# Performance work log

Measured on AMD Instinct MI355X. Metric: run time of the kernel, lower is better.

Reference implementation:

```python
import jax, jax.numpy as jnp
import numpy as np

T, H, I, E, K = 4096, 2048, 1408, 8, 2


def setup_inputs() -> dict:
    key = jax.random.key(0)
    k1, k2, k3, k4, k5 = jax.random.split(key, 5)
    hidden_states = jax.random.normal(k1, (T, H), dtype=jnp.float32)
    w13 = jax.random.normal(k2, (E, 2 * I, H), dtype=jnp.float32) * 0.02
    w2 = jax.random.normal(k3, (E, H, I), dtype=jnp.float32) * 0.02
    topk_ids = jax.random.randint(k4, (T, K), 0, E, dtype=jnp.int32)
    topk_weights = jax.random.uniform(k5, (T, K), dtype=jnp.float32)
    return {
        "hidden_states": hidden_states,
        "w13": w13,
        "w2": w2,
        "topk_ids": topk_ids,
        "topk_weights": topk_weights,
    }


def reference(hidden_states, w13, w2, topk_ids, topk_weights):
    # hidden_states: [T, H]; w13: [E, 2I, H]; w2: [E, H, I]
    # topk_ids/topk_weights: [T, K]. local_expert_start = 0.
    num_tokens, hidden = hidden_states.shape
    num_experts = w13.shape[0]
    inter = w13.shape[1] // 2
    gate_w = w13[:, :inter, :]  # [E, I, H]
    up_w = w13[:, inter:, :]    # [E, I, H]

    # Dense per-expert gate/up projections (vectorized grouped GEMM).
    gate = jnp.einsum('th,eih->tei', hidden_states, gate_w)
    up = jnp.einsum('th,eih->tei', hidden_states, up_w)
    act = jax.nn.silu(gate) * up  # [T, E, I]

    # Scatter topk weights into a dense [T, E] routing matrix (zero elsewhere),
    # which reproduces the trivial impl's per-slot weighted accumulation.
    tok = jnp.arange(num_tokens, dtype=jnp.int32)[:, None]
    routing = jnp.zeros((num_tokens, num_experts), dtype=hidden_states.dtype)
    routing = routing.at[tok, topk_ids].add(topk_weights)

    # Weighted combine through the down projection; weighting act first avoids
    # materializing a [T, E, H] intermediate.
    act_w = act * routing[:, :, None]  # [T, E, I]
    out = jnp.einsum('tei,ehi->th', act_w, w2)  # [T, H]
    return out
```

## Files before the change

kernel.cpp:

```cpp
#include <hip/hip_runtime.h>
#include <hip/hip_bf16.h>

#define T_TOK 4096
#define HID   2048
#define INTER 1408
#define TWO_I 2816
#define NEXP  8
#define ROWCAP 9216

#define N8_HS  1048576
#define N8_W13 5767168
#define NCVT   ((N8_HS + N8_W13) / 256)

using bf16x8 = __attribute__((ext_vector_type(8))) __bf16;
using f32x4  = __attribute__((ext_vector_type(4))) float;

__device__ __forceinline__ unsigned short f2bf(float f) {
  unsigned u = __float_as_uint(f);
  u += 0x7fffu + ((u >> 16) & 1u);
  return (unsigned short)(u >> 16);
}

__device__ __forceinline__ void gload16(const void* g, void* l) {
  __builtin_amdgcn_global_load_lds(
      (const __attribute__((address_space(1))) void*)g,
      (__attribute__((address_space(3))) void*)l, 16, 0, 0);
}

__device__ __forceinline__ uint4 pack8(float4 a, float4 b) {
  union { unsigned short us[8]; uint4 v; } o;
  o.us[0] = f2bf(a.x); o.us[1] = f2bf(a.y); o.us[2] = f2bf(a.z); o.us[3] = f2bf(a.w);
  o.us[4] = f2bf(b.x); o.us[5] = f2bf(b.y); o.us[6] = f2bf(b.z); o.us[7] = f2bf(b.w);
  return o.v;
}

__global__ void cvt2route_kernel(const float* __restrict__ hs_f, unsigned short* __restrict__ hs_b,
                                 const float* __restrict__ w13_f, unsigned short* __restrict__ w13_b,
                                 const int* __restrict__ ids, const float* __restrict__ wts,
                                 float* __restrict__ R, int* __restrict__ counts) {
  int bid = blockIdx.x;
  if (bid >= NCVT) {
    int t = (bid - NCVT) * 256 + threadIdx.x;
    if (t >= T_TOK) return;
    int e0 = ids[t * 2], e1 = ids[t * 2 + 1];
    float w0 = wts[t * 2], w1 = wts[t * 2 + 1];
#pragma unroll
    for (int ee = 0; ee < NEXP; ++ee) {
      float r = (e0 == ee ? w0 : 0.0f) + (e1 == ee ? w1 : 0.0f);
      R[t * NEXP + ee] = r;
    }
    atomicAdd(&counts[e0], 1);
    if (e1 != e0) atomicAdd(&counts[e1], 1);
    return;
  }
  int i = bid * 256 + threadIdx.x;
  const float4* p;
  uint4* o;
  int j;
  if (i < N8_HS) {
    p = reinterpret_cast<const float4*>(hs_f);
    o = reinterpret_cast<uint4*>(hs_b);
    j = i;
  } else {
    p = reinterpret_cast<const float4*>(w13_f);
    o = reinterpret_cast<uint4*>(w13_b);
    j = i - N8_HS;
  }
  o[j] = pack8(p[j * 2], p[j * 2 + 1]);
}

__global__ void offsets_kernel(const int* __restrict__ counts,
                               int* __restrict__ offs, int* __restrict__ cursor,
                               int* __restrict__ tl) {
  if (threadIdx.x == 0) {
    int o = 0;
    for (int e = 0; e < NEXP; ++e) {
      offs[e] = o;
      cursor[e] = o;
      o += (counts[e] + 127) & ~127;
    }
    offs[NEXP] = o;
  }
  for (int i = threadIdx.x; i < ROWCAP; i += 256) tl[i] = -1;
}

__global__ void scatter_kernel(const int* __restrict__ ids,
                               int* __restrict__ cursor, int* __restrict__ tl,
                               int* __restrict__ inv) {
  int t = blockIdx.x * 256 + threadIdx.x;
  if (t >= T_TOK) return;
  int e0 = ids[t * 2], e1 = ids[t * 2 + 1];
  int p = atomicAdd(&cursor[e0], 1);
  tl[p] = t;
  inv[t * 2] = p;
  if (e1 != e0) {
    p = atomicAdd(&cursor[e1], 1);
    tl[p] = t;
    inv[t * 2 + 1] = p;
  } else {
    inv[t * 2 + 1] = -1;
  }
}


#define BARR do { __asm__ __volatile__("" ::: "memory"); \
                  __builtin_amdgcn_s_barrier();           \
                  __asm__ __volatile__("" ::: "memory"); } while (0)
#define VMC(n) __asm__ __volatile__("s_waitcnt vmcnt(" #n ")" ::: "memory")

#define STG(P, h, kt, slotOff, hOff)                                        \
  do {                                                                      \
    gload16(P[h][0] + (kt) * 128, smem + (slotOff) + (hOff) + chA);         \
    gload16(P[h][1] + (kt) * 128, smem + (slotOff) + (hOff) + chA + 1024);  \
  } while (0)

#define LDA(dst, S, aq)                                                     \
  do {                                                                      \
    _Pragma("unroll") for (int mi = 0; mi < 4; ++mi) {                      \
      const char* _p = smem + (S) + wmOff + ((aq) * 64 + mi * 16 + l15) * 128; \
      dst[mi][0] = *(const bf16x8*)(_p + ko0);                              \
      dst[mi][1] = *(const bf16x8*)(_p + ko1);                              \
    }                                                                       \
  } while (0)

#define LDB(dst, S, bq)                                                     \
  do {                                                                      \
    _Pragma("unroll") for (int ni = 0; ni < 2; ++ni) {                      \
      const char* _p = smem + (S) + 32768 + wnhOff +                        \
                       (wn1 * 64 + ((bq) * 2 + ni) * 16 + l15) * 128;       \
      dst[ni][0] = *(const bf16x8*)(_p + ko0);                              \
      dst[ni][1] = *(const bf16x8*)(_p + ko1);                              \
    }                                                                       \
  } while (0)

#define MFQ(A, B, aq, bq)                                                   \
  do {                                                                      \
    __builtin_amdgcn_s_setprio(1);                                          \
    _Pragma("unroll") for (int mi = 0; mi < 4; ++mi)                        \
    _Pragma("unroll") for (int ni = 0; ni < 2; ++ni) {                      \
      acc[(aq) * 4 + mi][(bq) * 2 + ni] = __builtin_amdgcn_mfma_f32_16x16x32_bf16( \
          A[mi][0], B[ni][0], acc[(aq) * 4 + mi][(bq) * 2 + ni], 0, 0, 0);  \
      acc[(aq) * 4 + mi][(bq) * 2 + ni] = __builtin_amdgcn_mfma_f32_16x16x32_bf16( \
          A[mi][1], B[ni][1], acc[(aq) * 4 + mi][(bq) * 2 + ni], 0, 0, 0);  \
    }                                                                       \
    __builtin_amdgcn_s_setprio(0);                                          \
  } while (0)

#define EIGHT_PHASES(NIT_, NL_LIM_)                                         \
  for (int i = 0; i < (NIT_); ++i) {                                        \
    const int t0 = 2 * i, t1 = t0 + 1;                                      \
    const bool nl = (i < (NL_LIM_));                                        \
                                                                    \
    LDA(a_lo, 0, 0);                                                        \
    LDB(b_lo, 0, 0);                                                        \
    STG(aS, 0, t1, 65536, 0);                                               \
    BARR; MFQ(a_lo, b_lo, 0, 0); BARR;                                      \
                                                                    \
    LDB(b_hi, 0, 1);                                                        \
    STG(aS, 1, t1, 65536, 16384);                                           \
    BARR; MFQ(a_lo, b_hi, 0, 1); BARR;                                      \
                                                                    \
    LDA(a_hi, 0, 1);                                                        \
    if (nl) STG(bS, 0, t0 + 2, 0, 32768);                                   \
    BARR; MFQ(a_hi, b_hi, 1, 1); BARR;                                      \
                                                                    \
    if (nl) STG(bS, 1, t0 + 2, 0, 49152);                                   \
    BARR; MFQ(a_hi, b_lo, 1, 0);                                            \
    if (nl) { VMC(4); } else { VMC(0); }                                    \
    BARR;                                                                   \
                                                                    \
    LDA(a_lo, 65536, 0);                                                    \
    LDB(b_lo, 65536, 0);                                                    \
    if (nl) STG(aS, 0, t0 + 2, 0, 0);                                       \
    BARR; MFQ(a_lo, b_lo, 0, 0); BARR;                                      \
                                                                    \
    LDB(b_hi, 65536, 1);                                                    \
    if (nl) STG(aS, 1, t0 + 2, 0, 16384);                                   \
    BARR; MFQ(a_lo, b_hi, 0, 1); BARR;                                      \
                                                                    \
    LDA(a_hi, 65536, 1);                                                    \
    if (nl) STG(bS, 0, t1 + 2, 65536, 32768);                               \
    BARR; MFQ(a_hi, b_hi, 1, 1); BARR;                                      \
                                                                    \
    if (nl) STG(bS, 1, t1 + 2, 65536, 49152);                               \
    BARR; MFQ(a_hi, b_lo, 1, 0);                                            \
    if (nl) VMC(4);                                                         \
    BARR;                                                                   \
  }

#define PROLOGUE_STAGE()                                                    \
  do {                                                                      \
    STG(aS, 0, 0, 0, 0);                                                    \
    STG(aS, 1, 0, 0, 16384);                                                \
    STG(bS, 0, 0, 0, 32768);                                                \
    STG(bS, 1, 0, 0, 49152);                                                \
    STG(bS, 0, 1, 65536, 32768);                                            \
    STG(bS, 1, 1, 65536, 49152);                                            \
    VMC(4);                                                                 \
    BARR;                                                                   \
  } while (0)

__global__ __launch_bounds__(512, 2) void gemm1_kernel(
    const unsigned short* __restrict__ hs,
    const unsigned short* __restrict__ w13,
    unsigned short* __restrict__ act,
    const int* __restrict__ tl, const int* __restrict__ offs,
    const float* __restrict__ w2f, unsigned short* __restrict__ w2b) {
  const int tid = threadIdx.x;
  const int lin = blockIdx.x + 11 * (blockIdx.y + 16 * blockIdx.z);

  {
    const float4* p = reinterpret_cast<const float4*>(w2f);
    uint4* o = reinterpret_cast<uint4*>(w2b);
    int gid = lin * 512 + tid;
#pragma unroll
    for (int q = 0; q < 4; ++q) {
      int idx = q * 720896 + gid;
      o[idx] = pack8(p[idx * 2], p[idx * 2 + 1]);
    }
  }

  const int work = (lin & 7) * 176 + (lin >> 3);
  const int bz = work / 176;
  const int rem = work - bz * 176;
  const int bx = rem % 11;
  const int by = rem / 11;

  const int e = bz;
  const int rbeg = offs[e], rend = offs[e + 1];
  const int m0 = rbeg + by * 256;
  if (m0 >= rend) return;
  const int n0 = bx * 128;

  __shared__ __align__(16) char smem[131072];

  const int lane = tid & 63, wave = tid >> 6;
  const int wm = wave >> 2, wn = wave & 3;
  const int l15 = lane & 15;
  const int srow = lane >> 3;
  const int scolswz = ((lane & 7) * 16) ^ (srow << 4);
  const int chA = wave * 2048;
  const int wmOff = wm * 16384;
  const int wnhOff = (wn >> 1) * 16384;
  const int wn1 = wn & 1;
  const int rsw = (lane & 7) << 4;
  const int ko0 = ((lane >> 4) * 16) ^ rsw;
  const int ko1 = (64 + (lane >> 4) * 16) ^ rsw;

  const char* hs_b = (const char*)hs;
  const char* w13_b = (const char*)w13 + (size_t)e * (TWO_I * HID * 2);

  const char* aS[2][2];
  const char* bS[2][2];
#pragma unroll
  for (int h = 0; h < 2; ++h)
#pragma unroll
    for (int it = 0; it < 2; ++it) {
      int rl = h * 128 + (wave * 2 + it) * 8 + srow;
      int grow = m0 + rl;
      int tk = (grow < rend) ? tl[grow] : 0;
      if (tk < 0) tk = 0;
      aS[h][it] = hs_b + (size_t)tk * 4096 + scolswz;
      int wg = rl >> 6, sub = rl & 63;
      int srcB = (sub < 32) ? (n0 + wg * 32 + sub)
                            : (INTER + n0 + wg * 32 + (sub - 32));
      bS[h][it] = w13_b + (size_t)srcB * 4096 + scolswz;
    }

  f32x4 acc[8][4] = {};
  bf16x8 a_lo[4][2], a_hi[4][2], b_lo[2][2], b_hi[2][2];

  PROLOGUE_STAGE();
  EIGHT_PHASES(16, 15);

  const bool okst = (wm == 0) || (rend - m0 >= 256);
  if (okst) {
#pragma unroll
    for (int MI = 0; MI < 8; ++MI)
#pragma unroll
      for (int j = 0; j < 4; ++j) {
        int row = m0 + wm * 128 + MI * 16 + (lane >> 4) * 4 + j;
        size_t base = (size_t)row * INTER + n0 + wn * 32;
#pragma unroll
        for (int NI = 0; NI < 2; ++NI) {
          float g = acc[MI][NI][j], u = acc[MI][NI + 2][j];
          float s = (g / (1.0f + __expf(-g))) * u;
          act[base + NI * 16 + l15] = f2bf(s);
        }
      }
  }
}

__global__ __launch_bounds__(512, 2) void gemm2_kernel(
    const unsigned short* __restrict__ act,
    const unsigned short* __restrict__ w2,
    const float* __restrict__ R, const int* __restrict__ tl,
    const int* __restrict__ offs, unsigned short* __restrict__ partial) {
  const int tid = threadIdx.x;
  const int lin = blockIdx.x + 8 * (blockIdx.y + 16 * blockIdx.z);
  const int work = (lin & 7) * 128 + (lin >> 3);
  const int bz = work >> 7;
  const int rem = work & 127;
  const int bx = rem & 7;
  const int by = rem >> 3;

  const int e = bz;
  const int rbeg = offs[e], rend = offs[e + 1];
  const int m0 = rbeg + by * 256;
  if (m0 >= rend) return;
  const int n0 = bx * 256;

  __shared__ __align__(16) char smem[131072];

  const int lane = tid & 63, wave = tid >> 6;
  const int wm = wave >> 2, wn = wave & 3;
  const int l15 = lane & 15;
  const int srow = lane >> 3;
  const int scolswz = ((lane & 7) * 16) ^ (srow << 4);
  const int chA = wave * 2048;
  const int wmOff = wm * 16384;
  const int wnhOff = (wn >> 1) * 16384;
  const int wn1 = wn & 1;
  const int rsw = (lane & 7) << 4;
  const int ko0 = ((lane >> 4) * 16) ^ rsw;
  const int ko1 = (64 + (lane >> 4) * 16) ^ rsw;

  const char* act_b = (const char*)act;
  const char* w2_b = (const char*)w2 + (size_t)e * (HID * INTER * 2);

  const char* aS[2][2];
  const char* bS[2][2];
#pragma unroll
  for (int h = 0; h < 2; ++h)
#pragma unroll
    for (int it = 0; it < 2; ++it) {
      int rl = h * 128 + (wave * 2 + it) * 8 + srow;
      int grow = m0 + rl;
      if (grow >= rend) grow = rbeg;
      aS[h][it] = act_b + (size_t)grow * (INTER * 2) + scolswz;
      bS[h][it] = w2_b + (size_t)(n0 + rl) * (INTER * 2) + scolswz;
    }

  f32x4 acc[8][4] = {};
  bf16x8 a_lo[4][2], a_hi[4][2], b_lo[2][2], b_hi[2][2];

  PROLOGUE_STAGE();
  EIGHT_PHASES(11, 10);

  const bool okst = (wm == 0) || (rend - m0 >= 256);
  if (okst) {
#pragma unroll
    for (int MI = 0; MI < 8; ++MI) {
      float sc[4];
#pragma unroll
      for (int j = 0; j < 4; ++j) {
        int row = m0 + wm * 128 + MI * 16 + (lane >> 4) * 4 + j;
        int t = tl[row];
        sc[j] = t >= 0 ? R[t * NEXP + e] : 0.0f;
      }
#pragma unroll
      for (int NI = 0; NI < 4; ++NI) {
        int col = n0 + wn * 64 + NI * 16 + l15;
#pragma unroll
        for (int j = 0; j < 4; ++j) {
          int row = m0 + wm * 128 + MI * 16 + (lane >> 4) * 4 + j;
          partial[(size_t)row * HID + col] = f2bf(acc[MI][NI][j] * sc[j]);
        }
      }
    }
  }
}

__global__ void combine_kernel(const unsigned short* __restrict__ P,
                               const int* __restrict__ inv,
                               float* __restrict__ out) {
  int idx = blockIdx.x * 256 + threadIdx.x;
  int t = idx >> 8;
  int c = (idx & 255) << 3;
  int p0 = inv[t * 2], p1 = inv[t * 2 + 1];
  union { uint4 v; unsigned short us[8]; } a, b;
  a.v = *(const uint4*)(P + (size_t)p0 * HID + c);
  float f[8];
#pragma unroll
  for (int j = 0; j < 8; ++j) f[j] = __uint_as_float((unsigned)a.us[j] << 16);
  if (p1 >= 0) {
    b.v = *(const uint4*)(P + (size_t)p1 * HID + c);
#pragma unroll
    for (int j = 0; j < 8; ++j) f[j] += __uint_as_float((unsigned)b.us[j] << 16);
  }
  float4 lo = {f[0], f[1], f[2], f[3]}, hi = {f[4], f[5], f[6], f[7]};
  *(float4*)(out + (size_t)t * HID + c) = lo;
  *(float4*)(out + (size_t)t * HID + c + 4) = hi;
}

extern "C" void kernel_launch(void* const* d_in, const int* in_sizes, int n_in,
                              void* d_out, int out_size, void* d_ws, size_t ws_size,
                              hipStream_t stream) {
  const float* hs_f  = (const float*)d_in[0];
  const float* w13_f = (const float*)d_in[1];
  const float* w2_f  = (const float*)d_in[2];
  const int*   ids   = (const int*)d_in[3];
  const float* wts   = (const float*)d_in[4];
  float* out = (float*)d_out;
  char* ws = (char*)d_ws;

  unsigned short* hs_b  = (unsigned short*)(ws);
  unsigned short* w13_b = (unsigned short*)(ws + 16777216);
  unsigned short* w2_b  = (unsigned short*)(ws + 109051904);
  unsigned short* act   = (unsigned short*)(ws + 155189248);
  float* R              = (float*)(ws + 181141504);
  int*   tl             = (int*)(ws + 181272576);
  int*   inv            = (int*)(ws + 181309440);
  int*   meta           = (int*)(ws + 181342208);
  unsigned short* partial = (unsigned short*)(ws + 16777216);
  int* counts = meta;
  int* offs   = meta + 8;
  int* cursor = meta + 17;

  hipMemsetAsync(meta, 0, 32 * sizeof(int), stream);

  cvt2route_kernel<<<dim3(NCVT + 16), dim3(256), 0, stream>>>(
      hs_f, hs_b, w13_f, w13_b, ids, wts, R, counts);

  offsets_kernel<<<dim3(1), dim3(256), 0, stream>>>(counts, offs, cursor, tl);
  scatter_kernel<<<dim3(T_TOK / 256), dim3(256), 0, stream>>>(ids, cursor, tl, inv);

  gemm1_kernel<<<dim3(11, 16, 8), dim3(512), 0, stream>>>(hs_b, w13_b, act, tl, offs, w2_f, w2_b);
  gemm2_kernel<<<dim3(8, 16, 8), dim3(512), 0, stream>>>(act, w2_b, R, tl, offs, partial);
  combine_kernel<<<dim3(T_TOK * (HID / 8) / 256), dim3(256), 0, stream>>>(partial, inv, out);
}
```

Measured before the change: 299.6 us.

## Use persistent GEMM blocks with an atomic work queue for tile scheduling

Both grouped GEMM kernels now launch 256 persistent blocks instead of one block per potential tile. Each block pulls tile indices from a global atomic counter and skips tiles that lie past an expert's row range. This avoids launching and retiring the many empty tiles and balances work dynamically. The w2 fp32-to-bf16 conversion is redistributed over the 256 blocks. In exchange it adds two barriers per job, loses the previous expert-interleaved tile ordering (jobs now go in expert-major order), and may lower occupancy headroom.

```diff
diff --git a/kernel.cpp b/kernel.cpp
--- a/kernel.cpp
+++ b/kernel.cpp
@@ -11,6 +11,9 @@
 #define N8_HS  1048576
 #define N8_W13 5767168
 #define NCVT   ((N8_HS + N8_W13) / 256)
+
+#define NJOBS1 1408
+#define NJOBS2 1024
 
 using bf16x8 = __attribute__((ext_vector_type(8))) __bf16;
 using f32x4  = __attribute__((ext_vector_type(4))) float;
@@ -205,34 +208,23 @@
     const unsigned short* __restrict__ w13,
     unsigned short* __restrict__ act,
     const int* __restrict__ tl, const int* __restrict__ offs,
-    const float* __restrict__ w2f, unsigned short* __restrict__ w2b) {
+    const float* __restrict__ w2f, unsigned short* __restrict__ w2b,
+    int* __restrict__ qcnt) {
   const int tid = threadIdx.x;
-  const int lin = blockIdx.x + 11 * (blockIdx.y + 16 * blockIdx.z);
 
   {
     const float4* p = reinterpret_cast<const float4*>(w2f);
     uint4* o = reinterpret_cast<uint4*>(w2b);
-    int gid = lin * 512 + tid;
-#pragma unroll
-    for (int q = 0; q < 4; ++q) {
-      int idx = q * 720896 + gid;
+    int gid = blockIdx.x * 512 + tid;
+#pragma unroll
+    for (int q = 0; q < 22; ++q) {
+      int idx = q * 131072 + gid;
       o[idx] = pack8(p[idx * 2], p[idx * 2 + 1]);
     }
   }
 
-  const int work = (lin & 7) * 176 + (lin >> 3);
-  const int bz = work / 176;
-  const int rem = work - bz * 176;
-  const int bx = rem % 11;
-  const int by = rem / 11;
-
-  const int e = bz;
-  const int rbeg = offs[e], rend = offs[e + 1];
-  const int m0 = rbeg + by * 256;
-  if (m0 >= rend) return;
-  const int n0 = bx * 128;
-
   __shared__ __align__(16) char smem[131072];
+  __shared__ int sjob;
 
   const int lane = tid & 63, wave = tid >> 6;
   const int wm = wave >> 2, wn = wave & 3;
@@ -248,46 +240,65 @@
   const int ko1 = (64 + (lane >> 4) * 16) ^ rsw;
 
   const char* hs_b = (const char*)hs;
-  const char* w13_b = (const char*)w13 + (size_t)e * (TWO_I * HID * 2);
-
-  const char* aS[2][2];
-  const char* bS[2][2];
-#pragma unroll
-  for (int h = 0; h < 2; ++h)
-#pragma unroll
-    for (int it = 0; it < 2; ++it) {
-      int rl = h * 128 + (wave * 2 + it) * 8 + srow;
-      int grow = m0 + rl;
-      int tk = (grow < rend) ? tl[grow] : 0;
-      if (tk < 0) tk = 0;
-      aS[h][it] = hs_b + (size_t)tk * 4096 + scolswz;
-      int wg = rl >> 6, sub = rl & 63;
-      int srcB = (sub < 32) ? (n0 + wg * 32 + sub)
-                            : (INTER + n0 + wg * 32 + (sub - 32));
-      bS[h][it] = w13_b + (size_t)srcB * 4096 + scolswz;
+
+  for (;;) {
+    if (tid == 0) sjob = atomicAdd(qcnt, 1);
+    __syncthreads();
+    const int job = sjob;
+    __syncthreads();
+    if (job >= NJOBS1) break;
+
+    const int e = job / 176;
+    const int rem = job - e * 176;
+    const int by = rem / 11;
+    const int bx = rem - by * 11;
+
+    const int rbeg = offs[e], rend = offs[e + 1];
+    const int m0 = rbeg + by * 256;
+    if (m0 >= rend) continue;
+    const int n0 = bx * 128;
+
+    const char* w13_b = (const char*)w13 + (size_t)e * (TWO_I * HID * 2);
+
+    const char* aS[2][2];
+    const char* bS[2][2];
+#pragma unroll
+    for (int h = 0; h < 2; ++h)
+#pragma unroll
+      for (int it = 0; it < 2; ++it) {
+        int rl = h * 128 + (wave * 2 + it) * 8 + srow;
+        int grow = m0 + rl;
+        int tk = (grow < rend) ? tl[grow] : 0;
+        if (tk < 0) tk = 0;
+        aS[h][it] = hs_b + (size_t)tk * 4096 + scolswz;
+        int wg = rl >> 6, sub = rl & 63;
+        int srcB = (sub < 32) ? (n0 + wg * 32 + sub)
+                              : (INTER + n0 + wg * 32 + (sub - 32));
+        bS[h][it] = w13_b + (size_t)srcB * 4096 + scolswz;
+      }
+
+    f32x4 acc[8][4] = {};
+    bf16x8 a_lo[4][2], a_hi[4][2], b_lo[2][2], b_hi[2][2];
+
+    PROLOGUE_STAGE();
+    EIGHT_PHASES(16, 15);
+
+    const bool okst = (wm == 0) || (rend - m0 >= 256);
+    if (okst) {
+#pragma unroll
+      for (int MI = 0; MI < 8; ++MI)
+#pragma unroll
+        for (int j = 0; j < 4; ++j) {
+          int row = m0 + wm * 128 + MI * 16 + (lane >> 4) * 4 + j;
+          size_t base = (size_t)row * INTER + n0 + wn * 32;
+#pragma unroll
+          for (int NI = 0; NI < 2; ++NI) {
+            float g = acc[MI][NI][j], u = acc[MI][NI + 2][j];
+            float s = (g / (1.0f + __expf(-g))) * u;
+            act[base + NI * 16 + l15] = f2bf(s);
+          }
+        }
     }
-
-  f32x4 acc[8][4] = {};
-  bf16x8 a_lo[4][2], a_hi[4][2], b_lo[2][2], b_hi[2][2];
-
-  PROLOGUE_STAGE();
-  EIGHT_PHASES(16, 15);
-
-  const bool okst = (wm == 0) || (rend - m0 >= 256);
-  if (okst) {
-#pragma unroll
-    for (int MI = 0; MI < 8; ++MI)
-#pragma unroll
-      for (int j = 0; j < 4; ++j) {
-        int row = m0 + wm * 128 + MI * 16 + (lane >> 4) * 4 + j;
-        size_t base = (size_t)row * INTER + n0 + wn * 32;
-#pragma unroll
-        for (int NI = 0; NI < 2; ++NI) {
-          float g = acc[MI][NI][j], u = acc[MI][NI + 2][j];
-          float s = (g / (1.0f + __expf(-g))) * u;
-          act[base + NI * 16 + l15] = f2bf(s);
-        }
-      }
   }
 }
 
@@ -295,22 +306,12 @@
     const unsigned short* __restrict__ act,
     const unsigned short* __restrict__ w2,
     const float* __restrict__ R, const int* __restrict__ tl,
-    const int* __restrict__ offs, unsigned short* __restrict__ partial) {
+    const int* __restrict__ offs, unsigned short* __restrict__ partial,
+    int* __restrict__ qcnt) {
   const int tid = threadIdx.x;
-  const int lin = blockIdx.x + 8 * (blockIdx.y + 16 * blockIdx.z);
-  const int work = (lin & 7) * 128 + (lin >> 3);
-  const int bz = work >> 7;
-  const int rem = work & 127;
-  const int bx = rem & 7;
-  const int by = rem >> 3;
-
-  const int e = bz;
-  const int rbeg = offs[e], rend = offs[e + 1];
-  const int m0 = rbeg + by * 256;
-  if (m0 >= rend) return;
-  const int n0 = bx * 256;
 
   __shared__ __align__(16) char smem[131072];
+  __shared__ int sjob;
 
   const int lane = tid & 63, wave = tid >> 6;
   const int wm = wave >> 2, wn = wave & 3;
@@ -326,45 +327,64 @@
   const int ko1 = (64 + (lane >> 4) * 16) ^ rsw;
 
   const char* act_b = (const char*)act;
-  const char* w2_b = (const char*)w2 + (size_t)e * (HID * INTER * 2);
-
-  const char* aS[2][2];
-  const char* bS[2][2];
-#pragma unroll
-  for (int h = 0; h < 2; ++h)
-#pragma unroll
-    for (int it = 0; it < 2; ++it) {
-      int rl = h * 128 + (wave * 2 + it) * 8 + srow;
-      int grow = m0 + rl;
-      if (grow >= rend) grow = rbeg;
-      aS[h][it] = act_b + (size_t)grow * (INTER * 2) + scolswz;
-      bS[h][it] = w2_b + (size_t)(n0 + rl) * (INTER * 2) + scolswz;
-    }
-
-  f32x4 acc[8][4] = {};
-  bf16x8 a_lo[4][2], a_hi[4][2], b_lo[2][2], b_hi[2][2];
-
-  PROLOGUE_STAGE();
-  EIGHT_PHASES(11, 10);
-
-  const bool okst = (wm == 0) || (rend - m0 >= 256);
-  if (okst) {
-#pragma unroll
-    for (int MI = 0; MI < 8; ++MI) {
-      float sc[4];
-#pragma unroll
-      for (int j = 0; j < 4; ++j) {
-        int row = m0 + wm * 128 + MI * 16 + (lane >> 4) * 4 + j;
-        int t = tl[row];
-        sc[j] = t >= 0 ? R[t * NEXP + e] : 0.0f;
+
+  for (;;) {
+    if (tid == 0) sjob = atomicAdd(qcnt, 1);
+    __syncthreads();
+    const int job = sjob;
+    __syncthreads();
+    if (job >= NJOBS2) break;
+
+    const int e = job >> 7;
+    const int rem = job & 127;
+    const int by = rem >> 3;
+    const int bx = rem & 7;
+
+    const int rbeg = offs[e], rend = offs[e + 1];
+    const int m0 = rbeg + by * 256;
+    if (m0 >= rend) continue;
+    const int n0 = bx * 256;
+
+    const char* w2_b = (const char*)w2 + (size_t)e * (HID * INTER * 2);
+
+    const char* aS[2][2];
+    const char* bS[2][2];
+#pragma unroll
+    for (int h = 0; h < 2; ++h)
+#pragma unroll
+      for (int it = 0; it < 2; ++it) {
+        int rl = h * 128 + (wave * 2 + it) * 8 + srow;
+        int grow = m0 + rl;
+        if (grow >= rend) grow = rbeg;
+        aS[h][it] = act_b + (size_t)grow * (INTER * 2) + scolswz;
+        bS[h][it] = w2_b + (size_t)(n0 + rl) * (INTER * 2) + scolswz;
       }
-#pragma unroll
-      for (int NI = 0; NI < 4; ++NI) {
-        int col = n0 + wn * 64 + NI * 16 + l15;
+
+    f32x4 acc[8][4] = {};
+    bf16x8 a_lo[4][2], a_hi[4][2], b_lo[2][2], b_hi[2][2];
+
+    PROLOGUE_STAGE();
+    EIGHT_PHASES(11, 10);
+
+    const bool okst = (wm == 0) || (rend - m0 >= 256);
+    if (okst) {
+#pragma unroll
+      for (int MI = 0; MI < 8; ++MI) {
+        float sc[4];
 #pragma unroll
         for (int j = 0; j < 4; ++j) {
           int row = m0 + wm * 128 + MI * 16 + (lane >> 4) * 4 + j;
-          partial[(size_t)row * HID + col] = f2bf(acc[MI][NI][j] * sc[j]);
+          int t = tl[row];
+          sc[j] = t >= 0 ? R[t * NEXP + e] : 0.0f;
+        }
+#pragma unroll
+        for (int NI = 0; NI < 4; ++NI) {
+          int col = n0 + wn * 64 + NI * 16 + l15;
+#pragma unroll
+          for (int j = 0; j < 4; ++j) {
+            int row = m0 + wm * 128 + MI * 16 + (lane >> 4) * 4 + j;
+            partial[(size_t)row * HID + col] = f2bf(acc[MI][NI][j] * sc[j]);
+          }
         }
       }
     }
@@ -416,6 +436,8 @@
   int* counts = meta;
   int* offs   = meta + 8;
   int* cursor = meta + 17;
+  int* q1     = meta + 26;
+  int* q2     = meta + 27;
 
   hipMemsetAsync(meta, 0, 32 * sizeof(int), stream);
 
@@ -425,7 +447,7 @@
   offsets_kernel<<<dim3(1), dim3(256), 0, stream>>>(counts, offs, cursor, tl);
   scatter_kernel<<<dim3(T_TOK / 256), dim3(256), 0, stream>>>(ids, cursor, tl, inv);
 
-  gemm1_kernel<<<dim3(11, 16, 8), dim3(512), 0, stream>>>(hs_b, w13_b, act, tl, offs, w2_f, w2_b);
-  gemm2_kernel<<<dim3(8, 16, 8), dim3(512), 0, stream>>>(act, w2_b, R, tl, offs, partial);
+  gemm1_kernel<<<dim3(256), dim3(512), 0, stream>>>(hs_b, w13_b, act, tl, offs, w2_f, w2_b, q1);
+  gemm2_kernel<<<dim3(256), dim3(512), 0, stream>>>(act, w2_b, R, tl, offs, partial, q2);
   combine_kernel<<<dim3(T_TOK * (HID / 8) / 256), dim3(256), 0, stream>>>(partial, inv, out);
 }
```

Measured after the change: 356.3 us. 1.19x slower.

## Convert fp32 weights to bf16 inside GEMM loaders instead of separate pass

Applied to the files above, without the earlier changes.

Removes the standalone w13 and w2 fp32-to-bf16 conversion passes and instead has both GEMM kernels load fp32 weight tiles into registers, pack them to bf16 and write them to LDS. This eliminates writing and re-reading a bf16 weight copy in the workspace. In exchange, each GEMM tile reads twice the bytes for B, and the pipeline now waits for all outstanding loads each half-iteration, reducing overlap. It also shrinks the workspace layout.

```diff
diff --git a/kernel.cpp b/kernel.cpp
--- a/kernel.cpp
+++ b/kernel.cpp
@@ -9,8 +9,7 @@
 #define ROWCAP 9216
 
 #define N8_HS  1048576
-#define N8_W13 5767168
-#define NCVT   ((N8_HS + N8_W13) / 256)
+#define NCVT_HS (N8_HS / 256)
 
 using bf16x8 = __attribute__((ext_vector_type(8))) __bf16;
 using f32x4  = __attribute__((ext_vector_type(4))) float;
@@ -35,12 +34,11 @@
 }
 
 __global__ void cvt2route_kernel(const float* __restrict__ hs_f, unsigned short* __restrict__ hs_b,
-                                 const float* __restrict__ w13_f, unsigned short* __restrict__ w13_b,
                                  const int* __restrict__ ids, const float* __restrict__ wts,
                                  float* __restrict__ R, int* __restrict__ counts) {
   int bid = blockIdx.x;
-  if (bid >= NCVT) {
-    int t = (bid - NCVT) * 256 + threadIdx.x;
+  if (bid >= NCVT_HS) {
+    int t = (bid - NCVT_HS) * 256 + threadIdx.x;
     if (t >= T_TOK) return;
     int e0 = ids[t * 2], e1 = ids[t * 2 + 1];
     float w0 = wts[t * 2], w1 = wts[t * 2 + 1];
@@ -53,19 +51,9 @@
     if (e1 != e0) atomicAdd(&counts[e1], 1);
     return;
   }
-  int i = bid * 256 + threadIdx.x;
-  const float4* p;
-  uint4* o;
-  int j;
-  if (i < N8_HS) {
-    p = reinterpret_cast<const float4*>(hs_f);
-    o = reinterpret_cast<uint4*>(hs_b);
-    j = i;
-  } else {
-    p = reinterpret_cast<const float4*>(w13_f);
-    o = reinterpret_cast<uint4*>(w13_b);
-    j = i - N8_HS;
-  }
+  int j = bid * 256 + threadIdx.x;
+  const float4* p = reinterpret_cast<const float4*>(hs_f);
+  uint4* o = reinterpret_cast<uint4*>(hs_b);
   o[j] = pack8(p[j * 2], p[j * 2 + 1]);
 }
 
@@ -107,30 +95,32 @@
                   __builtin_amdgcn_s_barrier();           \
                   __asm__ __volatile__("" ::: "memory"); } while (0)
 #define VMC(n) __asm__ __volatile__("s_waitcnt vmcnt(" #n ")" ::: "memory")
-
-#define STG(P, h, kt, slotOff, hOff)                                        \
-  do {                                                                      \
-    gload16(P[h][0] + (kt) * 128, smem + (slotOff) + (hOff) + chA);         \
-    gload16(P[h][1] + (kt) * 128, smem + (slotOff) + (hOff) + chA + 1024);  \
-  } while (0)
-
-#define LDA(dst, S, aq)                                                     \
-  do {                                                                      \
-    _Pragma("unroll") for (int mi = 0; mi < 4; ++mi) {                      \
-      const char* _p = smem + (S) + wmOff + ((aq) * 64 + mi * 16 + l15) * 128; \
-      dst[mi][0] = *(const bf16x8*)(_p + ko0);                              \
-      dst[mi][1] = *(const bf16x8*)(_p + ko1);                              \
-    }                                                                       \
-  } while (0)
-
-#define LDB(dst, S, bq)                                                     \
-  do {                                                                      \
-    _Pragma("unroll") for (int ni = 0; ni < 2; ++ni) {                      \
-      const char* _p = smem + (S) + 32768 + wnhOff +                        \
-                       (wn1 * 64 + ((bq) * 2 + ni) * 16 + l15) * 128;       \
-      dst[ni][0] = *(const bf16x8*)(_p + ko0);                              \
-      dst[ni][1] = *(const bf16x8*)(_p + ko1);                              \
-    }                                                                       \
+#define LGKM0  __asm__ __volatile__("s_waitcnt lgkmcnt(0)" ::: "memory")
+
+#define STG_A(h, kt, slotOff, hOff)                                         \
+  do {                                                                      \
+    gload16(aS[h][0] + (kt) * 128, smem + (slotOff) + (hOff) + chA);        \
+    gload16(aS[h][1] + (kt) * 128, smem + (slotOff) + (hOff) + chA + 1024); \
+  } while (0)
+
+#define BISSUE(kt)                                                          \
+  do {                                                                      \
+    bv0[0] = *(const float4*)(bSf[0][0] + (kt) * 256);                      \
+    bv0[1] = *(const float4*)(bSf[0][0] + (kt) * 256 + 16);                 \
+    bv0[2] = *(const float4*)(bSf[0][1] + (kt) * 256);                      \
+    bv0[3] = *(const float4*)(bSf[0][1] + (kt) * 256 + 16);                 \
+    bv1[0] = *(const float4*)(bSf[1][0] + (kt) * 256);                      \
+    bv1[1] = *(const float4*)(bSf[1][0] + (kt) * 256 + 16);                 \
+    bv1[2] = *(const float4*)(bSf[1][1] + (kt) * 256);                      \
+    bv1[3] = *(const float4*)(bSf[1][1] + (kt) * 256 + 16);                 \
+  } while (0)
+
+#define BWRITE(dst, slotOff, hOff)                                          \
+  do {                                                                      \
+    *(uint4*)(smem + (slotOff) + (hOff) + chA + lane * 16) =                \
+        pack8(dst[0], dst[1]);                                              \
+    *(uint4*)(smem + (slotOff) + (hOff) + chA + 1024 + lane * 16) =         \
+        pack8(dst[2], dst[3]);                                              \
   } while (0)
 
 #define MFQ(A, B, aq, bq)                                                   \
@@ -146,79 +136,87 @@
     __builtin_amdgcn_s_setprio(0);                                          \
   } while (0)
 
-#define EIGHT_PHASES(NIT_, NL_LIM_)                                         \
+#define LDA(dst, S, aq)                                                     \
+  do {                                                                      \
+    _Pragma("unroll") for (int mi = 0; mi < 4; ++mi) {                      \
+      const char* _p = smem + (S) + wmOff + ((aq) * 64 + mi * 16 + l15) * 128; \
+      dst[mi][0] = *(const bf16x8*)(_p + ko0);                              \
+      dst[mi][1] = *(const bf16x8*)(_p + ko1);                              \
+    }                                                                       \
+  } while (0)
+
+#define LDB(dst, S, bq)                                                     \
+  do {                                                                      \
+    _Pragma("unroll") for (int ni = 0; ni < 2; ++ni) {                      \
+      const char* _p = smem + (S) + 32768 + wnhOff +                        \
+                       (wn1 * 64 + ((bq) * 2 + ni) * 16 + l15) * 128;       \
+      dst[ni][0] = *(const bf16x8*)(_p + ko0);                              \
+      dst[ni][1] = *(const bf16x8*)(_p + ko1);                              \
+    }                                                                       \
+  } while (0)
+
+#define EIGHT_PHASES_F(NIT_, NL_LIM_)                                       \
   for (int i = 0; i < (NIT_); ++i) {                                        \
     const int t0 = 2 * i, t1 = t0 + 1;                                      \
     const bool nl = (i < (NL_LIM_));                                        \
                                                                     \
     LDA(a_lo, 0, 0);                                                        \
     LDB(b_lo, 0, 0);                                                        \
-    STG(aS, 0, t1, 65536, 0);                                               \
+    STG_A(0, t1, 65536, 0);                                                 \
+    if (nl) { BISSUE(t0 + 2); }                                             \
     BARR; MFQ(a_lo, b_lo, 0, 0); BARR;                                      \
                                                                     \
     LDB(b_hi, 0, 1);                                                        \
-    STG(aS, 1, t1, 65536, 16384);                                           \
+    STG_A(1, t1, 65536, 16384);                                             \
     BARR; MFQ(a_lo, b_hi, 0, 1); BARR;                                      \
                                                                     \
     LDA(a_hi, 0, 1);                                                        \
-    if (nl) STG(bS, 0, t0 + 2, 0, 32768);                                   \
+    if (nl) { BWRITE(bv0, 0, 32768); BWRITE(bv1, 0, 49152); }               \
     BARR; MFQ(a_hi, b_hi, 1, 1); BARR;                                      \
                                                                     \
-    if (nl) STG(bS, 1, t0 + 2, 0, 49152);                                   \
+    VMC(0);                                                                 \
     BARR; MFQ(a_hi, b_lo, 1, 0);                                            \
-    if (nl) { VMC(4); } else { VMC(0); }                                    \
+    LGKM0;                                                                  \
     BARR;                                                                   \
                                                                     \
     LDA(a_lo, 65536, 0);                                                    \
     LDB(b_lo, 65536, 0);                                                    \
-    if (nl) STG(aS, 0, t0 + 2, 0, 0);                                       \
+    if (nl) { STG_A(0, t0 + 2, 0, 0); BISSUE(t1 + 2); }                     \
     BARR; MFQ(a_lo, b_lo, 0, 0); BARR;                                      \
                                                                     \
     LDB(b_hi, 65536, 1);                                                    \
-    if (nl) STG(aS, 1, t0 + 2, 0, 16384);                                   \
+    if (nl) { STG_A(1, t0 + 2, 0, 16384); }                                 \
     BARR; MFQ(a_lo, b_hi, 0, 1); BARR;                                      \
                                                                     \
     LDA(a_hi, 65536, 1);                                                    \
-    if (nl) STG(bS, 0, t1 + 2, 65536, 32768);                               \
+    if (nl) { BWRITE(bv0, 65536, 32768); BWRITE(bv1, 65536, 49152); }       \
     BARR; MFQ(a_hi, b_hi, 1, 1); BARR;                                      \
                                                                     \
-    if (nl) STG(bS, 1, t1 + 2, 65536, 49152);                               \
+    VMC(0);                                                                 \
     BARR; MFQ(a_hi, b_lo, 1, 0);                                            \
-    if (nl) VMC(4);                                                         \
+    LGKM0;                                                                  \
     BARR;                                                                   \
   }
 
-#define PROLOGUE_STAGE()                                                    \
-  do {                                                                      \
-    STG(aS, 0, 0, 0, 0);                                                    \
-    STG(aS, 1, 0, 0, 16384);                                                \
-    STG(bS, 0, 0, 0, 32768);                                                \
-    STG(bS, 1, 0, 0, 49152);                                                \
-    STG(bS, 0, 1, 65536, 32768);                                            \
-    STG(bS, 1, 1, 65536, 49152);                                            \
-    VMC(4);                                                                 \
-    BARR;                                                                   \
+#define PROLOGUE_F()                                                        \
+  do {                                                                      \
+    STG_A(0, 0, 0, 0); STG_A(1, 0, 0, 16384);                               \
+    BISSUE(0);                                                              \
+    VMC(0);                                                                 \
+    BWRITE(bv0, 0, 32768); BWRITE(bv1, 0, 49152);                           \
+    BISSUE(1);                                                              \
+    VMC(0);                                                                 \
+    BWRITE(bv0, 65536, 32768); BWRITE(bv1, 65536, 49152);                   \
+    LGKM0; BARR;                                                            \
   } while (0)
 
 __global__ __launch_bounds__(512, 2) void gemm1_kernel(
     const unsigned short* __restrict__ hs,
-    const unsigned short* __restrict__ w13,
+    const float* __restrict__ w13f,
     unsigned short* __restrict__ act,
-    const int* __restrict__ tl, const int* __restrict__ offs,
-    const float* __restrict__ w2f, unsigned short* __restrict__ w2b) {
+    const int* __restrict__ tl, const int* __restrict__ offs) {
   const int tid = threadIdx.x;
   const int lin = blockIdx.x + 11 * (blockIdx.y + 16 * blockIdx.z);
-
-  {
-    const float4* p = reinterpret_cast<const float4*>(w2f);
-    uint4* o = reinterpret_cast<uint4*>(w2b);
-    int gid = lin * 512 + tid;
-#pragma unroll
-    for (int q = 0; q < 4; ++q) {
-      int idx = q * 720896 + gid;
-      o[idx] = pack8(p[idx * 2], p[idx * 2 + 1]);
-    }
-  }
 
   const int work = (lin & 7) * 176 + (lin >> 3);
   const int bz = work / 176;
@@ -248,10 +246,9 @@
   const int ko1 = (64 + (lane >> 4) * 16) ^ rsw;
 
   const char* hs_b = (const char*)hs;
-  const char* w13_b = (const char*)w13 + (size_t)e * (TWO_I * HID * 2);
 
   const char* aS[2][2];
-  const char* bS[2][2];
+  const char* bSf[2][2];
 #pragma unroll
   for (int h = 0; h < 2; ++h)
 #pragma unroll
@@ -264,14 +261,15 @@
       int wg = rl >> 6, sub = rl & 63;
       int srcB = (sub < 32) ? (n0 + wg * 32 + sub)
                             : (INTER + n0 + wg * 32 + (sub - 32));
-      bS[h][it] = w13_b + (size_t)srcB * 4096 + scolswz;
+      bSf[h][it] = (const char*)w13f + ((size_t)e * TWO_I + srcB) * (HID * 4) + scolswz * 2;
     }
 
   f32x4 acc[8][4] = {};
   bf16x8 a_lo[4][2], a_hi[4][2], b_lo[2][2], b_hi[2][2];
-
-  PROLOGUE_STAGE();
-  EIGHT_PHASES(16, 15);
+  float4 bv0[4], bv1[4];
+
+  PROLOGUE_F();
+  EIGHT_PHASES_F(16, 15);
 
   const bool okst = (wm == 0) || (rend - m0 >= 256);
   if (okst) {
@@ -293,7 +291,7 @@
 
 __global__ __launch_bounds__(512, 2) void gemm2_kernel(
     const unsigned short* __restrict__ act,
-    const unsigned short* __restrict__ w2,
+    const float* __restrict__ w2f,
     const float* __restrict__ R, const int* __restrict__ tl,
     const int* __restrict__ offs, unsigned short* __restrict__ partial) {
   const int tid = threadIdx.x;
@@ -326,10 +324,9 @@
   const int ko1 = (64 + (lane >> 4) * 16) ^ rsw;
 
   const char* act_b = (const char*)act;
-  const char* w2_b = (const char*)w2 + (size_t)e * (HID * INTER * 2);
 
   const char* aS[2][2];
-  const char* bS[2][2];
+  const char* bSf[2][2];
 #pragma unroll
   for (int h = 0; h < 2; ++h)
 #pragma unroll
@@ -338,14 +335,15 @@
       int grow = m0 + rl;
       if (grow >= rend) grow = rbeg;
       aS[h][it] = act_b + (size_t)grow * (INTER * 2) + scolswz;
-      bS[h][it] = w2_b + (size_t)(n0 + rl) * (INTER * 2) + scolswz;
+      bSf[h][it] = (const char*)w2f + ((size_t)e * HID + n0 + rl) * (INTER * 4) + scolswz * 2;
     }
 
   f32x4 acc[8][4] = {};
   bf16x8 a_lo[4][2], a_hi[4][2], b_lo[2][2], b_hi[2][2];
-
-  PROLOGUE_STAGE();
-  EIGHT_PHASES(11, 10);
+  float4 bv0[4], bv1[4];
+
+  PROLOGUE_F();
+  EIGHT_PHASES_F(11, 10);
 
   const bool okst = (wm == 0) || (rend - m0 >= 256);
   if (okst) {
@@ -404,28 +402,26 @@
   float* out = (float*)d_out;
   char* ws = (char*)d_ws;
 
-  unsigned short* hs_b  = (unsigned short*)(ws);
-  unsigned short* w13_b = (unsigned short*)(ws + 16777216);
-  unsigned short* w2_b  = (unsigned short*)(ws + 109051904);
-  unsigned short* act   = (unsigned short*)(ws + 155189248);
-  float* R              = (float*)(ws + 181141504);
-  int*   tl             = (int*)(ws + 181272576);
-  int*   inv            = (int*)(ws + 181309440);
-  int*   meta           = (int*)(ws + 181342208);
-  unsigned short* partial = (unsigned short*)(ws + 16777216);
+  unsigned short* hs_b    = (unsigned short*)(ws);
+  unsigned short* act     = (unsigned short*)(ws + 16777216);
+  unsigned short* partial = (unsigned short*)(ws + 42729472);
+  float* R                = (float*)(ws + 80478208);
+  int*   tl               = (int*)(ws + 80609280);
+  int*   inv              = (int*)(ws + 80646144);
+  int*   meta             = (int*)(ws + 80678912);
   int* counts = meta;
   int* offs   = meta + 8;
   int* cursor = meta + 17;
 
   hipMemsetAsync(meta, 0, 32 * sizeof(int), stream);
 
-  cvt2route_kernel<<<dim3(NCVT + 16), dim3(256), 0, stream>>>(
-      hs_f, hs_b, w13_f, w13_b, ids, wts, R, counts);
+  cvt2route_kernel<<<dim3(NCVT_HS + 16), dim3(256), 0, stream>>>(
+      hs_f, hs_b, ids, wts, R, counts);
 
   offsets_kernel<<<dim3(1), dim3(256), 0, stream>>>(counts, offs, cursor, tl);
   scatter_kernel<<<dim3(T_TOK / 256), dim3(256), 0, stream>>>(ids, cursor, tl, inv);
 
-  gemm1_kernel<<<dim3(11, 16, 8), dim3(512), 0, stream>>>(hs_b, w13_b, act, tl, offs, w2_f, w2_b);
-  gemm2_kernel<<<dim3(8, 16, 8), dim3(512), 0, stream>>>(act, w2_b, R, tl, offs, partial);
+  gemm1_kernel<<<dim3(11, 16, 8), dim3(512), 0, stream>>>(hs_b, w13_f, act, tl, offs);
+  gemm2_kernel<<<dim3(8, 16, 8), dim3(512), 0, stream>>>(act, w2_f, R, tl, offs, partial);
   combine_kernel<<<dim3(T_TOK * (HID / 8) / 256), dim3(256), 0, stream>>>(partial, inv, out);
 }
```

Result: slower. 441.6 us (+47.4%).
